# Performance work log

Hardware: AMD Instinct MI355X
Metric: run time of the kernel (lower is better)

## Reference

```python
import jax, jax.numpy as jnp
import numpy as np

N = 1048576
DIM = 2
HID = 64
E = 4


def setup_inputs() -> dict:
    key = jax.random.key(0)
    ks = jax.random.split(key, 10)
    s_in = 1.0 / np.sqrt(DIM)
    s_hid = 1.0 / np.sqrt(HID)
    return {
        "x": jax.random.normal(ks[0], (N, DIM), dtype=jnp.float32),
        # router: Linear(dim -> E)
        "rW": jax.random.uniform(ks[1], (DIM, E), minval=-s_in, maxval=s_in, dtype=jnp.float32),
        "rb": jax.random.uniform(ks[2], (E,), minval=-s_in, maxval=s_in, dtype=jnp.float32),
        # stacked expert weights: Linear(dim->hid), Linear(hid->hid), Linear(hid->dim)
        "w1": jax.random.uniform(ks[3], (E, DIM, HID), minval=-s_in, maxval=s_in, dtype=jnp.float32),
        "b1": jax.random.uniform(ks[4], (E, HID), minval=-s_in, maxval=s_in, dtype=jnp.float32),
        "w2": jax.random.uniform(ks[5], (E, HID, HID), minval=-s_hid, maxval=s_hid, dtype=jnp.float32),
        "b2": jax.random.uniform(ks[6], (E, HID), minval=-s_hid, maxval=s_hid, dtype=jnp.float32),
        "w3": jax.random.uniform(ks[7], (E, HID, DIM), minval=-s_hid, maxval=s_hid, dtype=jnp.float32),
        "b3": jax.random.uniform(ks[8], (E, DIM), minval=-s_hid, maxval=s_hid, dtype=jnp.float32),
    }


def reference(x, rW, rb, w1, b1, w2, b2, w3, b3):
    # Router: hard top-1 via argmax, exactly as torch.argmax(router_logits, -1)
    router_logits = x @ rW + rb                       # [N, E]
    best = jnp.argmax(router_logits, axis=-1)         # [N]

    # Compute all experts densely (vectorized replacement of the masked loop),
    # then select the winning expert's output per token via one-hot.
    h = jax.nn.relu(jnp.einsum('nd,edh->enh', x, w1) + b1[:, None, :])   # [E, N, HID]
    h = jax.nn.relu(jnp.einsum('enh,ehk->enk', h, w2) + b2[:, None, :])  # [E, N, HID]
    y = jnp.einsum('enh,ehd->end', h, w3) + b3[:, None, :]               # [E, N, DIM]

    onehot = jax.nn.one_hot(best, E, dtype=x.dtype)   # [N, E]
    out = jnp.einsum('end,ne->nd', y, onehot)         # [N, DIM]
    return out, router_logits
```

## Files before the change

### kernel.cpp

```cpp
#include <hip/hip_runtime.h>

#define NTOK 1048576
#define HID 64
#define TPB 256
#define TPB_TOK 2048
#define RPT (TPB_TOK / TPB)
#define NBLK (NTOK / TPB_TOK)
#define MAXSLOT (TPB_TOK + 64)
#define MAXTILE (TPB_TOK / 16 + 4)

typedef _Float16 half8 __attribute__((ext_vector_type(8)));
typedef _Float16 half2v __attribute__((ext_vector_type(2)));
typedef float f32x4 __attribute__((ext_vector_type(4)));

static __device__ __forceinline__ half2v pkh(float a, float b) {
    return __builtin_bit_cast(half2v, __builtin_amdgcn_cvt_pkrtz(a, b));
}

__global__ void prep_w2_frag(const float* __restrict__ w2, _Float16* __restrict__ wsf) {
    int idx  = blockIdx.x * 256 + threadIdx.x;
    int j    = idx & 7;
    int lane = (idx >> 3) & 63;
    int ks   = (idx >> 9) & 1;
    int mt   = (idx >> 10) & 3;
    int e    = idx >> 12;
    int kin  = ks * 32 + (lane >> 4) * 8 + j;
    int m    = mt * 16 + (lane & 15);
    wsf[idx] = (_Float16)w2[(e * HID + kin) * HID + m];
}

__global__ __launch_bounds__(TPB, 2) void moe_kernel(
    const float* __restrict__ x, const float* __restrict__ rW, const float* __restrict__ rb,
    const float* __restrict__ w1, const float* __restrict__ b1,
    const float* __restrict__ b2,
    const float* __restrict__ w3, const float* __restrict__ b3,
    const _Float16* __restrict__ wsf, float* __restrict__ out)
{
    __shared__ float2 xs[MAXSLOT];
    __shared__ int ids[MAXSLOT];
    __shared__ int wcnt[4][4];
    __shared__ int seg_start[4], cnt_sh[4], cumt[5];
    __shared__ unsigned tmap[MAXTILE];

    const int t = threadIdx.x, w = t >> 6, lane = t & 63;
    const int base = blockIdx.x * TPB_TOK;
    const unsigned long long lt = (1ull << lane) - 1ull;

    const float r00 = rW[0], r01 = rW[1], r02 = rW[2], r03 = rW[3];
    const float r10 = rW[4], r11 = rW[5], r12 = rW[6], r13 = rW[7];
    const float rb0 = rb[0], rb1 = rb[1], rb2 = rb[2], rb3 = rb[3];

    int c0 = 0, c1 = 0, c2 = 0, c3 = 0;
    int slotl[RPT]; int bestl[RPT]; float2 xv_[RPT];
    float* logits_out = out + 2 * NTOK;
    #pragma unroll
    for (int i = 0; i < RPT; i++) {
        int tok = base + i * TPB + t;
        float2 xv = ((const float2*)x)[tok];
        float l0 = xv.x * r00 + xv.y * r10 + rb0;
        float l1 = xv.x * r01 + xv.y * r11 + rb1;
        float l2 = xv.x * r02 + xv.y * r12 + rb2;
        float l3 = xv.x * r03 + xv.y * r13 + rb3;
        ((float4*)logits_out)[tok] = make_float4(l0, l1, l2, l3);
        int b = 0; float bv = l0;
        if (l1 > bv) { bv = l1; b = 1; }
        if (l2 > bv) { bv = l2; b = 2; }
        if (l3 > bv) { bv = l3; b = 3; }
        unsigned long long m0 = __ballot(b == 0), m1 = __ballot(b == 1),
                           m2 = __ballot(b == 2), m3 = __ballot(b == 3);
        unsigned long long mym = (b == 0) ? m0 : (b == 1) ? m1 : (b == 2) ? m2 : m3;
        int cb = (b == 0) ? c0 : (b == 1) ? c1 : (b == 2) ? c2 : c3;
        slotl[i] = cb + __popcll(mym & lt);
        bestl[i] = b; xv_[i] = xv;
        c0 += __popcll(m0); c1 += __popcll(m1); c2 += __popcll(m2); c3 += __popcll(m3);
    }
    if (lane < 4) wcnt[w][lane] = (lane == 0) ? c0 : (lane == 1) ? c1 : (lane == 2) ? c2 : c3;
    __syncthreads();
    if (t == 0) {
        int run = 0, ct = 0; cumt[0] = 0;
        for (int e = 0; e < 4; e++) {
            int c = wcnt[0][e] + wcnt[1][e] + wcnt[2][e] + wcnt[3][e];
            cnt_sh[e] = c; seg_start[e] = run;
            run += (c + 15) & ~15; ct += (c + 15) >> 4; cumt[e + 1] = ct;
        }
    }
    __syncthreads();
    int wo0 = 0, wo1 = 0, wo2 = 0, wo3 = 0;
    for (int ww = 0; ww < w; ww++) {
        wo0 += wcnt[ww][0]; wo1 += wcnt[ww][1]; wo2 += wcnt[ww][2]; wo3 += wcnt[ww][3];
    }
    #pragma unroll
    for (int i = 0; i < RPT; i++) {
        int b = bestl[i];
        int wo = (b == 0) ? wo0 : (b == 1) ? wo1 : (b == 2) ? wo2 : wo3;
        int slot = seg_start[b] + wo + slotl[i];
        xs[slot] = xv_[i];
        ids[slot] = base + i * TPB + t;
    }
    int T = cumt[4];
    for (int g = t; g < T; g += TPB) {
        int e = (g >= cumt[1]) + (g >= cumt[2]) + (g >= cumt[3]);
        int i = g - cumt[e];
        int row = seg_start[e] + 16 * i;
        int cn = cnt_sh[e] - 16 * i; if (cn > 16) cn = 16;
        tmap[g] = (unsigned)e | ((unsigned)row << 2) | ((unsigned)cn << 18);
    }
    __syncthreads();

    const int q = lane >> 4, n16 = lane & 15;
    int chunk = (T + 3) >> 2;
    int g0 = w * chunk, g1 = g0 + chunk; if (g1 > T) g1 = T;

    half2v w1h0[8], w1h1[8], b1h[8];
    half8 w2A[4][2];
    float4 b2r[4], w3a[4], w3b[4];
    float2 b3r = make_float2(0.f, 0.f);
    int cur_e = -1;

    unsigned tm_n = 0; float2 xv_n = make_float2(0.f, 0.f); int id_n = 0;
    if (g0 < g1) {
        tm_n = tmap[g0];
        int r_ = (tm_n >> 2) & 0xFFF;
        xv_n = xs[r_ + n16];
        id_n = ids[r_ + n16];
    }

    for (int g = g0; g < g1; g++) {
        unsigned tm = tm_n; float2 xv = xv_n; int idv = id_n;
        if (g + 1 < g1) {
            tm_n = tmap[g + 1];
            int r_ = (tm_n >> 2) & 0xFFF;
            xv_n = xs[r_ + n16];
            id_n = ids[r_ + n16];
        }
        int e  = tm & 3;
        int cn = tm >> 18;
        if (e != cur_e) {
            cur_e = e;
            const float* base0 = w1 + e * 128;
            const float* base1 = w1 + e * 128 + 64;
            const float* baseb = b1 + e * 64;
            #pragma unroll
            for (int p = 0; p < 4; p++) {
                float2 a0 = *(const float2*)(base0 + q * 8 + 2 * p);
                float2 a1 = *(const float2*)(base0 + 32 + q * 8 + 2 * p);
                w1h0[p]     = pkh(a0.x, a0.y);
                w1h0[4 + p] = pkh(a1.x, a1.y);
                float2 c0_ = *(const float2*)(base1 + q * 8 + 2 * p);
                float2 c1_ = *(const float2*)(base1 + 32 + q * 8 + 2 * p);
                w1h1[p]     = pkh(c0_.x, c0_.y);
                w1h1[4 + p] = pkh(c1_.x, c1_.y);
                float2 d0 = *(const float2*)(baseb + q * 8 + 2 * p);
                float2 d1 = *(const float2*)(baseb + 32 + q * 8 + 2 * p);
                b1h[p]     = pkh(d0.x, d0.y);
                b1h[4 + p] = pkh(d1.x, d1.y);
            }
            #pragma unroll
            for (int mt = 0; mt < 4; mt++) {
                w2A[mt][0] = ((const half8*)wsf)[((e * 4 + mt) * 2 + 0) * 64 + lane];
                w2A[mt][1] = ((const half8*)wsf)[((e * 4 + mt) * 2 + 1) * 64 + lane];
                b2r[mt] = ((const float4*)(b2 + e * 64))[mt * 4 + q];
                w3a[mt] = ((const float4*)(w3 + e * 128))[mt * 8 + q * 2];
                w3b[mt] = ((const float4*)(w3 + e * 128))[mt * 8 + q * 2 + 1];
            }
            b3r = ((const float2*)b3)[e];
        }
        half2v xh0 = pkh(xv.x, xv.x);
        half2v xh1 = pkh(xv.y, xv.y);
        const half2v hz = { (_Float16)0, (_Float16)0 };
        half8 bf0, bf1;
        #pragma unroll
        for (int p = 0; p < 4; p++) {
            half2v ha = w1h0[p] * xh0 + w1h1[p] * xh1 + b1h[p];
            half2v hb = w1h0[4 + p] * xh0 + w1h1[4 + p] * xh1 + b1h[4 + p];
            ha = __builtin_elementwise_max(ha, hz);
            hb = __builtin_elementwise_max(hb, hz);
            bf0[2 * p] = ha.x; bf0[2 * p + 1] = ha.y;
            bf1[2 * p] = hb.x; bf1[2 * p + 1] = hb.y;
        }
        float y0m[4], y1m[4];
        #pragma unroll
        for (int mt = 0; mt < 4; mt++) {
            f32x4 acc = {0.f, 0.f, 0.f, 0.f};
            acc = __builtin_amdgcn_mfma_f32_16x16x32_f16(w2A[mt][0], bf0, acc, 0, 0, 0);
            acc = __builtin_amdgcn_mfma_f32_16x16x32_f16(w2A[mt][1], bf1, acc, 0, 0, 0);
            float4 bb = b2r[mt], wa = w3a[mt], wb = w3b[mt];
            float h, a0 = 0.f, a1 = 0.f;
            h = fmaxf(acc[0] + bb.x, 0.f); a0 = fmaf(h, wa.x, a0); a1 = fmaf(h, wa.y, a1);
            h = fmaxf(acc[1] + bb.y, 0.f); a0 = fmaf(h, wa.z, a0); a1 = fmaf(h, wa.w, a1);
            h = fmaxf(acc[2] + bb.z, 0.f); a0 = fmaf(h, wb.x, a0); a1 = fmaf(h, wb.y, a1);
            h = fmaxf(acc[3] + bb.w, 0.f); a0 = fmaf(h, wb.z, a0); a1 = fmaf(h, wb.w, a1);
            y0m[mt] = a0; y1m[mt] = a1;
        }
        float y0 = (y0m[0] + y0m[1]) + (y0m[2] + y0m[3]);
        float y1 = (y1m[0] + y1m[1]) + (y1m[2] + y1m[3]);
        y0 += __shfl_xor(y0, 16); y0 += __shfl_xor(y0, 32);
        y1 += __shfl_xor(y1, 16); y1 += __shfl_xor(y1, 32);
        if (q == 0 && n16 < cn) {
            ((float2*)out)[idv] = make_float2(y0 + b3r.x, y1 + b3r.y);
        }
    }
}

extern "C" void kernel_launch(void* const* d_in, const int* in_sizes, int n_in,
                              void* d_out, int out_size, void* d_ws, size_t ws_size,
                              hipStream_t stream) {
    const float* x  = (const float*)d_in[0];
    const float* rW = (const float*)d_in[1];
    const float* rb = (const float*)d_in[2];
    const float* w1 = (const float*)d_in[3];
    const float* b1 = (const float*)d_in[4];
    const float* w2 = (const float*)d_in[5];
    const float* b2 = (const float*)d_in[6];
    const float* w3 = (const float*)d_in[7];
    const float* b3 = (const float*)d_in[8];
    float* out = (float*)d_out;
    _Float16* wsf = (_Float16*)d_ws;

    hipLaunchKernelGGL(prep_w2_frag, dim3(64), dim3(256), 0, stream, w2, wsf);
    hipLaunchKernelGGL(moe_kernel, dim3(NBLK), dim3(TPB), 0, stream,
                       x, rW, rb, w1, b1, b2, w3, b3, (const _Float16*)wsf, out);
}
```

Measured before the change: 106.0 us.

## Use packed fp16 epilogue, stage outputs in LDS for coalesced stores, halve block tokens

The per-tile epilogue (bias2, ReLU, the w3 projection and the cross-lane reductions) now runs in packed half2 math instead of fp32. Tile outputs go to shared memory and are written back in original token order with coalesced stores, replacing scattered stores by token id. The block now handles 1024 tokens instead of 2048 and occupancy is raised to 4 blocks per CU. The goals are fewer ALU instructions, more coalesced global writes and more resident waves, at the cost of fp16 accumulation precision in the final projection.

```diff
diff --git a/kernel.cpp b/kernel.cpp
--- a/kernel.cpp
+++ b/kernel.cpp
@@ -3,7 +3,7 @@
 #define NTOK 1048576
 #define HID 64
 #define TPB 256
-#define TPB_TOK 2048
+#define TPB_TOK 1024
 #define RPT (TPB_TOK / TPB)
 #define NBLK (NTOK / TPB_TOK)
 #define MAXSLOT (TPB_TOK + 64)
@@ -29,7 +29,7 @@
     wsf[idx] = (_Float16)w2[(e * HID + kin) * HID + m];
 }
 
-__global__ __launch_bounds__(TPB, 2) void moe_kernel(
+__global__ __launch_bounds__(TPB, 4) void moe_kernel(
     const float* __restrict__ x, const float* __restrict__ rW, const float* __restrict__ rb,
     const float* __restrict__ w1, const float* __restrict__ b1,
     const float* __restrict__ b2,
@@ -37,9 +37,9 @@
     const _Float16* __restrict__ wsf, float* __restrict__ out)
 {
     __shared__ float2 xs[MAXSLOT];
-    __shared__ int ids[MAXSLOT];
+    __shared__ float2 ysh[MAXSLOT];
     __shared__ int wcnt[4][4];
-    __shared__ int seg_start[4], cnt_sh[4], cumt[5];
+    __shared__ int seg_start[4], cumt[5];
     __shared__ unsigned tmap[MAXTILE];
 
     const int t = threadIdx.x, w = t >> 6, lane = t & 63;
@@ -51,7 +51,7 @@
     const float rb0 = rb[0], rb1 = rb[1], rb2 = rb[2], rb3 = rb[3];
 
     int c0 = 0, c1 = 0, c2 = 0, c3 = 0;
-    int slotl[RPT]; int bestl[RPT]; float2 xv_[RPT];
+    int slotl[RPT]; int bestl[RPT]; float2 xv_[RPT]; int slotf[RPT];
     float* logits_out = out + 2 * NTOK;
     #pragma unroll
     for (int i = 0; i < RPT; i++) {
@@ -80,7 +80,7 @@
         int run = 0, ct = 0; cumt[0] = 0;
         for (int e = 0; e < 4; e++) {
             int c = wcnt[0][e] + wcnt[1][e] + wcnt[2][e] + wcnt[3][e];
-            cnt_sh[e] = c; seg_start[e] = run;
+            seg_start[e] = run;
             run += (c + 15) & ~15; ct += (c + 15) >> 4; cumt[e + 1] = ct;
         }
     }
@@ -95,15 +95,14 @@
         int wo = (b == 0) ? wo0 : (b == 1) ? wo1 : (b == 2) ? wo2 : wo3;
         int slot = seg_start[b] + wo + slotl[i];
         xs[slot] = xv_[i];
-        ids[slot] = base + i * TPB + t;
+        slotf[i] = slot;
     }
     int T = cumt[4];
     for (int g = t; g < T; g += TPB) {
         int e = (g >= cumt[1]) + (g >= cumt[2]) + (g >= cumt[3]);
         int i = g - cumt[e];
         int row = seg_start[e] + 16 * i;
-        int cn = cnt_sh[e] - 16 * i; if (cn > 16) cn = 16;
-        tmap[g] = (unsigned)e | ((unsigned)row << 2) | ((unsigned)cn << 18);
+        tmap[g] = (unsigned)e | ((unsigned)row << 2);
     }
     __syncthreads();
 
@@ -113,28 +112,26 @@
 
     half2v w1h0[8], w1h1[8], b1h[8];
     half8 w2A[4][2];
-    float4 b2r[4], w3a[4], w3b[4];
+    half2v b2h[4][2];
+    half2v w3h[4][4];
     float2 b3r = make_float2(0.f, 0.f);
     int cur_e = -1;
-
-    unsigned tm_n = 0; float2 xv_n = make_float2(0.f, 0.f); int id_n = 0;
+    const half2v hz = { (_Float16)0, (_Float16)0 };
+
+    unsigned tm_n = 0; float2 xv_n = make_float2(0.f, 0.f);
     if (g0 < g1) {
         tm_n = tmap[g0];
-        int r_ = (tm_n >> 2) & 0xFFF;
-        xv_n = xs[r_ + n16];
-        id_n = ids[r_ + n16];
+        xv_n = xs[((tm_n >> 2) & 0xFFF) + n16];
     }
 
     for (int g = g0; g < g1; g++) {
-        unsigned tm = tm_n; float2 xv = xv_n; int idv = id_n;
+        unsigned tm = tm_n; float2 xv = xv_n;
         if (g + 1 < g1) {
             tm_n = tmap[g + 1];
-            int r_ = (tm_n >> 2) & 0xFFF;
-            xv_n = xs[r_ + n16];
-            id_n = ids[r_ + n16];
-        }
-        int e  = tm & 3;
-        int cn = tm >> 18;
+            xv_n = xs[((tm_n >> 2) & 0xFFF) + n16];
+        }
+        int e   = tm & 3;
+        int row = (tm >> 2) & 0xFFF;
         if (e != cur_e) {
             cur_e = e;
             const float* base0 = w1 + e * 128;
@@ -159,15 +156,20 @@
             for (int mt = 0; mt < 4; mt++) {
                 w2A[mt][0] = ((const half8*)wsf)[((e * 4 + mt) * 2 + 0) * 64 + lane];
                 w2A[mt][1] = ((const half8*)wsf)[((e * 4 + mt) * 2 + 1) * 64 + lane];
-                b2r[mt] = ((const float4*)(b2 + e * 64))[mt * 4 + q];
-                w3a[mt] = ((const float4*)(w3 + e * 128))[mt * 8 + q * 2];
-                w3b[mt] = ((const float4*)(w3 + e * 128))[mt * 8 + q * 2 + 1];
+                float4 bb = ((const float4*)(b2 + e * 64))[mt * 4 + q];
+                b2h[mt][0] = pkh(bb.x, bb.y);
+                b2h[mt][1] = pkh(bb.z, bb.w);
+                #pragma unroll
+                for (int i = 0; i < 4; i++) {
+                    int r = mt * 16 + q * 4 + i;
+                    float2 wv = ((const float2*)(w3 + e * 128))[r];
+                    w3h[mt][i] = pkh(wv.x, wv.y);
+                }
             }
             b3r = ((const float2*)b3)[e];
         }
         half2v xh0 = pkh(xv.x, xv.x);
         half2v xh1 = pkh(xv.y, xv.y);
-        const half2v hz = { (_Float16)0, (_Float16)0 };
         half8 bf0, bf1;
         #pragma unroll
         for (int p = 0; p < 4; p++) {
@@ -178,27 +180,36 @@
             bf0[2 * p] = ha.x; bf0[2 * p + 1] = ha.y;
             bf1[2 * p] = hb.x; bf1[2 * p + 1] = hb.y;
         }
-        float y0m[4], y1m[4];
+        half2v ya = hz, yb = hz;
         #pragma unroll
         for (int mt = 0; mt < 4; mt++) {
             f32x4 acc = {0.f, 0.f, 0.f, 0.f};
             acc = __builtin_amdgcn_mfma_f32_16x16x32_f16(w2A[mt][0], bf0, acc, 0, 0, 0);
             acc = __builtin_amdgcn_mfma_f32_16x16x32_f16(w2A[mt][1], bf1, acc, 0, 0, 0);
-            float4 bb = b2r[mt], wa = w3a[mt], wb = w3b[mt];
-            float h, a0 = 0.f, a1 = 0.f;
-            h = fmaxf(acc[0] + bb.x, 0.f); a0 = fmaf(h, wa.x, a0); a1 = fmaf(h, wa.y, a1);
-            h = fmaxf(acc[1] + bb.y, 0.f); a0 = fmaf(h, wa.z, a0); a1 = fmaf(h, wa.w, a1);
-            h = fmaxf(acc[2] + bb.z, 0.f); a0 = fmaf(h, wb.x, a0); a1 = fmaf(h, wb.y, a1);
-            h = fmaxf(acc[3] + bb.w, 0.f); a0 = fmaf(h, wb.z, a0); a1 = fmaf(h, wb.w, a1);
-            y0m[mt] = a0; y1m[mt] = a1;
-        }
-        float y0 = (y0m[0] + y0m[1]) + (y0m[2] + y0m[3]);
-        float y1 = (y1m[0] + y1m[1]) + (y1m[2] + y1m[3]);
-        y0 += __shfl_xor(y0, 16); y0 += __shfl_xor(y0, 32);
-        y1 += __shfl_xor(y1, 16); y1 += __shfl_xor(y1, 32);
-        if (q == 0 && n16 < cn) {
-            ((float2*)out)[idv] = make_float2(y0 + b3r.x, y1 + b3r.y);
-        }
+            half2v h01 = __builtin_elementwise_max(pkh(acc[0], acc[1]) + b2h[mt][0], hz);
+            half2v h23 = __builtin_elementwise_max(pkh(acc[2], acc[3]) + b2h[mt][1], hz);
+            half2v h0s = { h01.x, h01.x }, h1s = { h01.y, h01.y };
+            half2v h2s = { h23.x, h23.x }, h3s = { h23.y, h23.y };
+            half2v* acc01 = (mt & 2) ? &yb : &ya;
+            *acc01 = *acc01 + h0s * w3h[mt][0];
+            *acc01 = *acc01 + h1s * w3h[mt][1];
+            *acc01 = *acc01 + h2s * w3h[mt][2];
+            *acc01 = *acc01 + h3s * w3h[mt][3];
+        }
+        half2v yp = ya + yb;
+        float yr = __builtin_bit_cast(float, yp);
+        yp = yp + __builtin_bit_cast(half2v, __shfl_xor(yr, 16));
+        yr = __builtin_bit_cast(float, yp);
+        yp = yp + __builtin_bit_cast(half2v, __shfl_xor(yr, 32));
+        if (q == 0) {
+            ysh[row + n16] = make_float2((float)yp.x + b3r.x, (float)yp.y + b3r.y);
+        }
+    }
+    __syncthreads();
+
+    #pragma unroll
+    for (int i = 0; i < RPT; i++) {
+        ((float2*)out)[base + i * TPB + t] = ysh[slotf[i]];
     }
 }
 
```

Result: faster. 103.1 us (median of 2 runs) (-2.7%).
